# Kernel optimization log

Hardware: AMD Instinct MI355X
Metric: run time of the kernel (lower is better)

## Reference

```python
import jax, jax.numpy as jnp
import numpy as np

BATCH, SEQ, IN_DIM = 4, 2048, 4
D_MODEL, HEADS, D_HEAD = 128, 8, 16
DEPTH, BUCKET, N_HASHES = 6, 64, 8
D_FF = 4 * D_MODEL
NUM_CLASSES = 2
NB = SEQ // BUCKET          # 32 buckets per hash round
SELF_ATTN_VALUE = -5e4      # lucidrains TOKEN_SELF_ATTN_VALUE


def setup_inputs() -> dict:
    key = jax.random.key(0)
    ks = jax.random.split(key, 12)
    rn = lambda k, s: jax.random.normal(k, s, jnp.float32) * 0.02
    return {
        "x": jax.random.normal(ks[0], (BATCH, SEQ, IN_DIM), jnp.float32),
        "emb_W": rn(ks[1], (IN_DIM, D_MODEL)),
        "emb_b": jnp.zeros((D_MODEL,), jnp.float32),
        "Wqk": rn(ks[2], (DEPTH, D_MODEL, D_MODEL)),
        "Wv": rn(ks[3], (DEPTH, D_MODEL, D_MODEL)),
        "Wo": rn(ks[4], (DEPTH, D_MODEL, D_MODEL)),
        "R": jax.random.normal(ks[5], (DEPTH, HEADS, D_HEAD, N_HASHES, NB // 2), jnp.float32),
        "ln1_g": jnp.ones((DEPTH, D_MODEL), jnp.float32),
        "ln1_b": jnp.zeros((DEPTH, D_MODEL), jnp.float32),
        "ln2_g": jnp.ones((DEPTH, D_MODEL), jnp.float32),
        "ln2_b": jnp.zeros((DEPTH, D_MODEL), jnp.float32),
        "ff_W1": rn(ks[6], (DEPTH, D_MODEL, D_FF)),
        "ff_b1": jnp.zeros((DEPTH, D_FF), jnp.float32),
        "ff_W2": rn(ks[7], (DEPTH, D_FF, D_MODEL)),
        "ff_b2": jnp.zeros((DEPTH, D_MODEL), jnp.float32),
        "fc_W": rn(ks[8], (D_MODEL, NUM_CLASSES)),
        "fc_b": jnp.zeros((NUM_CLASSES,), jnp.float32),
    }


def layer_norm(x, g, b, eps=1e-5):
    m = x.mean(-1, keepdims=True)
    v = ((x - m) ** 2).mean(-1, keepdims=True)
    return (x - m) * jax.lax.rsqrt(v + eps) * g + b


def lsh_attention(x, wqk, wv, wo, rot):
    # x: [B,S,D]; rot: [H, dh, n_hashes, NB//2]. Shared-QK LSH attention (eval mode, no dropout).
    B, S, D = x.shape
    qk = (x @ wqk).reshape(B, S, HEADS, D_HEAD).transpose(0, 2, 1, 3)  # [B,H,S,dh]
    v = (x @ wv).reshape(B, S, HEADS, D_HEAD).transpose(0, 2, 1, 3)

    # --- hashing: argmax over [xR; -xR] rotations ---
    rx = jnp.einsum('bhsd,hdnr->bhnsr', qk, rot)                # [B,H,n_hashes,S,NB/2]
    buckets = jnp.argmax(jnp.concatenate([rx, -rx], -1), -1)    # [B,H,n_hashes,S] in [0,NB)
    buckets = buckets + (jnp.arange(N_HASHES) * NB)[None, None, :, None]
    buckets = buckets.reshape(B, HEADS, N_HASHES * S)

    # --- stable sort by (bucket, position) ---
    ticker = jnp.arange(N_HASHES * S)
    sticker = jnp.argsort(buckets * S + (ticker % S), axis=-1)   # [B,H,L]
    undo = jnp.argsort(sticker, axis=-1)
    st = sticker % S                                              # original positions

    sqk = jnp.take_along_axis(qk, st[..., None], axis=2)          # [B,H,L,dh]
    sv = jnp.take_along_axis(v, st[..., None], axis=2)

    n_chunks = N_HASHES * NB
    bq = sqk.reshape(B, HEADS, n_chunks, BUCKET, D_HEAD)
    bk = bq / jnp.linalg.norm(bq, axis=-1, keepdims=True)         # shared-QK: keys are normalized queries
    bv = sv.reshape(B, HEADS, n_chunks, BUCKET, D_HEAD)
    bt = st.reshape(B, HEADS, n_chunks, BUCKET)

    look_back = lambda t: jnp.concatenate([t, jnp.roll(t, 1, axis=2)], axis=3)
    bk, bv, bkt = look_back(bk), look_back(bv), look_back(bt)

    dots = jnp.einsum('bhcid,bhcjd->bhcij', bq, bk) * (D_HEAD ** -0.5)  # [B,H,C,64,128]
    dots = jnp.where(bt[..., :, None] == bkt[..., None, :], SELF_ATTN_VALUE, dots)

    logsum = jax.nn.logsumexp(dots, axis=-1)                      # [B,H,C,64]
    probs = jnp.exp(dots - logsum[..., None])
    bo = jnp.einsum('bhcij,bhcjd->bhcid', probs, bv)

    so = bo.reshape(B, HEADS, N_HASHES * S, D_HEAD)
    slog = logsum.reshape(B, HEADS, N_HASHES * S)
    o = jnp.take_along_axis(so, undo[..., None], axis=2).reshape(B, HEADS, N_HASHES, S, D_HEAD)
    logits = jnp.take_along_axis(slog, undo, axis=2).reshape(B, HEADS, N_HASHES, S, 1)

    w = jax.nn.softmax(logits, axis=2)                            # combine hash rounds
    out = (o * w).sum(axis=2)                                     # [B,H,S,dh]
    out = out.transpose(0, 2, 1, 3).reshape(B, S, D)
    return out @ wo


def reference(x, emb_W, emb_b, Wqk, Wv, Wo, R, ln1_g, ln1_b, ln2_g, ln2_b,
              ff_W1, ff_b1, ff_W2, ff_b2, fc_W, fc_b):
    h = x @ emb_W + emb_b

    def layer(h, p):
        wqk, wv, wo, r, g1, b1g, g2, b2g, w1, bb1, w2, bb2 = p
        h = h + lsh_attention(layer_norm(h, g1, b1g), wqk, wv, wo, r)
        y = layer_norm(h, g2, b2g)
        h = h + (jax.nn.gelu(y @ w1 + bb1) @ w2 + bb2)
        return h, None

    h, _ = jax.lax.scan(layer, h, (Wqk, Wv, Wo, R, ln1_g, ln1_b, ln2_g, ln2_b,
                                   ff_W1, ff_b1, ff_W2, ff_b2))
    return h.mean(axis=1) @ fc_W + fc_b
```

## Files before the change

kernel.cpp:

```cpp
#include <hip/hip_runtime.h>
#include <math.h>

#define BB 4
#define SS 2048
#define INDIM 4
#define DD 128
#define HH 8
#define DH 16
#define DEPTH 6
#define BUCKET 64
#define NHASH 8
#define NBK 32
#define DFF 512
#define LL (NHASH*SS)
#define NCHUNK (NHASH*NBK)
#define NBH (BB*HH)

typedef short bf16x8 __attribute__((ext_vector_type(8)));
typedef _Float16 f16x8 __attribute__((ext_vector_type(8)));
typedef _Float16 f16x2 __attribute__((ext_vector_type(2)));
typedef float f32x4 __attribute__((ext_vector_type(4)));

__device__ __forceinline__ unsigned short f2bf(float f) {
    unsigned u = __builtin_bit_cast(unsigned, f);
    unsigned r = u + 0x7FFFu + ((u >> 16) & 1u);
    return (unsigned short)(r >> 16);
}

__global__ void k_embed(const float* __restrict__ x, const float* __restrict__ W,
                        const float* __restrict__ b, float* __restrict__ h) {
    int idx = blockIdx.x * blockDim.x + threadIdx.x;
    if (idx >= BB*SS*DD) return;
    int d = idx % DD, bs = idx / DD;
    const float* xr = x + bs*INDIM;
    float acc = b[d];
    #pragma unroll
    for (int k = 0; k < INDIM; k++) acc += xr[k] * W[k*DD + d];
    h[idx] = acc;
}

__global__ void k_wcast(const float* __restrict__ src, unsigned short* __restrict__ dst,
                        int R, int C) {
    __shared__ float tile[32][33];
    int l = blockIdx.z;
    const float* s = src + (size_t)l*R*C;
    unsigned short* d = dst + (size_t)l*R*C;
    int c0 = blockIdx.x*32, r0 = blockIdx.y*32;
    int tx = threadIdx.x, ty = threadIdx.y;
    #pragma unroll
    for (int i = 0; i < 4; i++)
        tile[ty + i*8][tx] = s[(size_t)(r0 + ty + i*8)*C + c0 + tx];
    __syncthreads();
    #pragma unroll
    for (int i = 0; i < 4; i++)
        d[(size_t)(c0 + ty + i*8)*R + r0 + tx] = f2bf(tile[tx][ty + i*8]);
}

__global__ void k_wcast16(const float* __restrict__ src, _Float16* __restrict__ dst,
                          int R, int C) {
    __shared__ float tile[32][33];
    int l = blockIdx.z;
    const float* s = src + (size_t)l*R*C;
    _Float16* d = dst + (size_t)l*R*C;
    int c0 = blockIdx.x*32, r0 = blockIdx.y*32;
    int tx = threadIdx.x, ty = threadIdx.y;
    #pragma unroll
    for (int i = 0; i < 4; i++)
        tile[ty + i*8][tx] = s[(size_t)(r0 + ty + i*8)*C + c0 + tx];
    __syncthreads();
    #pragma unroll
    for (int i = 0; i < 4; i++)
        d[(size_t)(c0 + ty + i*8)*R + r0 + tx] = (_Float16)tile[tx][ty + i*8];
}

__global__ __launch_bounds__(256, 4)
void k_proj_qkv(const float* __restrict__ hin, const float* __restrict__ lng,
                const float* __restrict__ lnb, const _Float16* __restrict__ WqkT,
                const _Float16* __restrict__ WvT, float* __restrict__ qk,
                _Float16* __restrict__ kn16, _Float16* __restrict__ v16,
                float* __restrict__ nrmg) {
    __shared__ float A[16][128];
    __shared__ __align__(16) _Float16 Lf[16][136];
    int row0 = blockIdx.x * 16;
    int t = threadIdx.x;
    {
        const float4* src = (const float4*)(hin + (size_t)row0*DD);
        float4* dst = (float4*)&A[0][0];
        dst[t]       = src[t];
        dst[t + 256] = src[t + 256];
    }
    __syncthreads();
    {
        int r = t >> 4, sub = t & 15;
        float4 xa = *(const float4*)&A[r][sub*8];
        float4 xb = *(const float4*)&A[r][sub*8 + 4];
        float s = xa.x+xa.y+xa.z+xa.w + xb.x+xb.y+xb.z+xb.w;
        s += __shfl_xor(s,1); s += __shfl_xor(s,2);
        s += __shfl_xor(s,4); s += __shfl_xor(s,8);
        float m = s * (1.0f/128.0f);
        float d0=xa.x-m, d1=xa.y-m, d2=xa.z-m, d3=xa.w-m;
        float d4=xb.x-m, d5=xb.y-m, d6=xb.z-m, d7=xb.w-m;
        float vs = d0*d0+d1*d1+d2*d2+d3*d3+d4*d4+d5*d5+d6*d6+d7*d7;
        vs += __shfl_xor(vs,1); vs += __shfl_xor(vs,2);
        vs += __shfl_xor(vs,4); vs += __shfl_xor(vs,8);
        float inv = 1.0f / sqrtf(vs * (1.0f/128.0f) + 1e-5f);
        float4 ga = *(const float4*)&lng[sub*8], gb = *(const float4*)&lng[sub*8+4];
        float4 ba = *(const float4*)&lnb[sub*8], bb = *(const float4*)&lnb[sub*8+4];
        f16x8 vv;
        vv[0] = (_Float16)(d0*inv*ga.x + ba.x);
        vv[1] = (_Float16)(d1*inv*ga.y + ba.y);
        vv[2] = (_Float16)(d2*inv*ga.z + ba.z);
        vv[3] = (_Float16)(d3*inv*ga.w + ba.w);
        vv[4] = (_Float16)(d4*inv*gb.x + bb.x);
        vv[5] = (_Float16)(d5*inv*gb.y + bb.y);
        vv[6] = (_Float16)(d6*inv*gb.z + bb.z);
        vv[7] = (_Float16)(d7*inv*gb.w + bb.w);
        *(f16x8*)&Lf[r][sub*8] = vv;
    }
    __syncthreads();
    int w = t >> 6, lane = t & 63;
    int fr = lane & 15, kg = lane >> 4;
    f32x4 aq[2], av[2];
    aq[0] = (f32x4){0.f,0.f,0.f,0.f}; aq[1] = (f32x4){0.f,0.f,0.f,0.f};
    av[0] = (f32x4){0.f,0.f,0.f,0.f}; av[1] = (f32x4){0.f,0.f,0.f,0.f};
    #pragma unroll
    for (int ks = 0; ks < 4; ks++) {
        f16x8 af = *(const f16x8*)&Lf[fr][ks*32 + kg*8];
        #pragma unroll
        for (int nt = 0; nt < 2; nt++) {
            const _Float16* bp = WqkT + (size_t)(w*32 + nt*16 + fr)*128 + ks*32 + kg*8;
            f16x8 bq = *(const f16x8*)bp;
            aq[nt] = __builtin_amdgcn_mfma_f32_16x16x32_f16(af, bq, aq[nt], 0, 0, 0);
            const _Float16* vp = WvT + (size_t)(w*32 + nt*16 + fr)*128 + ks*32 + kg*8;
            f16x8 bv = *(const f16x8*)vp;
            av[nt] = __builtin_amdgcn_mfma_f32_16x16x32_f16(af, bv, av[nt], 0, 0, 0);
        }
    }
    int b = row0 / SS;
    int sb = row0 & (SS-1);
    #pragma unroll
    for (int nt = 0; nt < 2; nt++) {
        int n = w*32 + nt*16 + fr;
        int h_ = n >> 4, d_ = n & 15;
        float ssq[4];
        #pragma unroll
        for (int i = 0; i < 4; i++) { float xx = aq[nt][i]; ssq[i] = xx*xx; }
        #pragma unroll
        for (int o = 1; o <= 8; o <<= 1) {
            #pragma unroll
            for (int i = 0; i < 4; i++) ssq[i] += __shfl_xor(ssq[i], o);
        }
        #pragma unroll
        for (int i = 0; i < 4; i++) {
            int s = sb + kg*4 + i;
            size_t rowi = ((size_t)(b*HH + h_))*SS + s;
            qk[rowi*DH + d_] = aq[nt][i];
            float nn = sqrtf(ssq[i]);
            float inv = 1.0f / nn;
            kn16[rowi*DH + d_] = (_Float16)(aq[nt][i] * inv);
            v16[rowi*DH + d_]  = (_Float16)(av[nt][i]);
            if (d_ == 0) nrmg[rowi] = nn * 0.25f * 1.4426950408889634f;
        }
    }
}

__global__ void k_hash(const float* __restrict__ qk, const float* __restrict__ R,
                       int* __restrict__ bkt) {
    __shared__ float Rs[256];
    int idx = blockIdx.x*256 + threadIdx.x;
    int s = idx & (SS-1); int t2 = idx >> 11;
    int n = t2 & 7; int bh = t2 >> 3; int h_ = bh & 7;
    {
        int tt = threadIdx.x;
        int d = tt >> 4, r = tt & 15;
        Rs[tt] = R[(((h_*DH + d)*NHASH + n)*16) + r];
    }
    __syncthreads();
    const float4* q4 = (const float4*)(qk + ((size_t)bh*SS + s)*DH);
    float4 q0 = q4[0], q1 = q4[1], q2 = q4[2], q3 = q4[3];
    float rxv[16];
    #pragma unroll
    for (int r = 0; r < 16; r++) {
        rxv[r] = q0.x*Rs[  0+r] + q0.y*Rs[ 16+r] + q0.z*Rs[ 32+r] + q0.w*Rs[ 48+r]
               + q1.x*Rs[ 64+r] + q1.y*Rs[ 80+r] + q1.z*Rs[ 96+r] + q1.w*Rs[112+r]
               + q2.x*Rs[128+r] + q2.y*Rs[144+r] + q2.z*Rs[160+r] + q2.w*Rs[176+r]
               + q3.x*Rs[192+r] + q3.y*Rs[208+r] + q3.z*Rs[224+r] + q3.w*Rs[240+r];
    }
    float best = rxv[0]; int bi = 0;
    #pragma unroll
    for (int jx = 1; jx < 16; jx++) if (rxv[jx]  > best) { best = rxv[jx];  bi = jx; }
    #pragma unroll
    for (int jx = 0; jx < 16; jx++) if (-rxv[jx] > best) { best = -rxv[jx]; bi = 16 + jx; }
    bkt[idx] = n*NBK + bi;
}

__global__ void k_scatter(const int* __restrict__ bkt, int* __restrict__ sticker) {
    __shared__ int hist[256*33];
    __shared__ int cs[8*33];
    __shared__ int bbk[NBK];
    int blk = blockIdx.x;
    int n = blk & 7, bh = blk >> 3;
    int t = threadIdx.x;
    #pragma unroll
    for (int k = 0; k < NBK; k++) hist[t*33 + k] = 0;
    const int* bp = bkt + (size_t)bh*LL + n*SS;
    int local[8];
    #pragma unroll
    for (int e = 0; e < 8; e++) {
        int k = bp[t*8 + e] - n*NBK;
        local[e] = k;
        hist[t*33 + k]++;
    }
    __syncthreads();
    {
        int i = t >> 5, k = t & 31;
        int ssum = 0;
        #pragma unroll
        for (int rr = 0; rr < 32; rr++) ssum += hist[(i*32+rr)*33 + k];
        cs[i*33 + k] = ssum;
    }
    __syncthreads();
    if (t < 32) {
        int tot = 0;
        #pragma unroll
        for (int i = 0; i < 8; i++) tot += cs[i*33 + t];
        int x = tot;
        #pragma unroll
        for (int o = 1; o < 32; o <<= 1) {
            int y = __shfl(x, (t >= o) ? (t - o) : 0, 64);
            if (t >= o) x += y;
        }
        bbk[t] = n*SS + x - tot;
    }
    __syncthreads();
    {
        int i = t >> 5, k = t & 31;
        int run = bbk[k];
        for (int ii = 0; ii < i; ii++) run += cs[ii*33 + k];
        for (int rr = 0; rr < 32; rr++) {
            int idx = (i*32+rr)*33 + k;
            int c0 = hist[idx];
            hist[idx] = run;
            run += c0;
        }
    }
    __syncthreads();
    #pragma unroll
    for (int e = 0; e < 8; e++) {
        int k = local[e];
        int pos = hist[t*33 + k]++;
        sticker[(size_t)bh*LL + pos] = n*SS + t*8 + e;
    }
}

__global__ __launch_bounds__(256, 4)
void k_attn(const _Float16* __restrict__ kn16, const _Float16* __restrict__ v16,
            const float* __restrict__ nrmg, const int* __restrict__ sticker,
            _Float16* __restrict__ so, float* __restrict__ slog) {
    __shared__ __align__(16) char smem[33024];
    _Float16 (*Kf)[40]  = (_Float16(*)[40])smem;
    _Float16 (*P)[136]  = (_Float16(*)[136])(smem + 10240);
    _Float16 (*VT)[136] = (_Float16(*)[136])(smem + 27648);
    int*   pk   = (int*)(smem + 32000);
    float* nrm  = (float*)(smem + 32512);
    int*   lraw = (int*)(smem + 32768);

    int blk = blockIdx.x;
    int c = blk & (NCHUNK-1), bh = blk >> 8;
    int t = threadIdx.x;
    const int* stk = sticker + (size_t)bh*LL;

    if (t < 128) {
        int j = t;
        int cc = (j < 64) ? c : ((c + NCHUNK - 1) & (NCHUNK-1));
        int raw = stk[cc*BUCKET + (j & 63)];
        int sk = raw & (SS-1);
        const f16x8* kp = (const f16x8*)(kn16 + ((size_t)bh*SS + sk)*DH);
        f16x8 z = {0,0,0,0,0,0,0,0};
        *(f16x8*)&Kf[j][0]  = kp[0];
        *(f16x8*)&Kf[j][8]  = kp[1];
        *(f16x8*)&Kf[j][16] = z;
        *(f16x8*)&Kf[j][24] = z;
        pk[j] = sk;
        if (j < 64) { nrm[j] = nrmg[(size_t)bh*SS + sk]; lraw[j] = raw; }
    } else {
        int j = t - 128;
        int cc = (j < 64) ? c : ((c + NCHUNK - 1) & (NCHUNK-1));
        int sk = stk[cc*BUCKET + (j & 63)] & (SS-1);
        const f16x8* vp = (const f16x8*)(v16 + ((size_t)bh*SS + sk)*DH);
        f16x8 v0 = vp[0], v1 = vp[1];
        VT[ 0][j]=v0[0]; VT[ 1][j]=v0[1]; VT[ 2][j]=v0[2]; VT[ 3][j]=v0[3];
        VT[ 4][j]=v0[4]; VT[ 5][j]=v0[5]; VT[ 6][j]=v0[6]; VT[ 7][j]=v0[7];
        VT[ 8][j]=v1[0]; VT[ 9][j]=v1[1]; VT[10][j]=v1[2]; VT[11][j]=v1[3];
        VT[12][j]=v1[4]; VT[13][j]=v1[5]; VT[14][j]=v1[6]; VT[15][j]=v1[7];
    }
    __syncthreads();

    int w = t >> 6, lane = t & 63;
    int fr = lane & 15, kg = lane >> 4;
    int qrow = w*16 + fr;

    f32x4 acc[8];
    #pragma unroll
    for (int nt = 0; nt < 8; nt++) acc[nt] = (f32x4){0.f,0.f,0.f,0.f};
    {
        f16x8 kfq = *(const f16x8*)&Kf[qrow][kg*8];
        _Float16 qs = (_Float16)nrm[qrow];
        f16x8 bq = kfq * qs;
        #pragma unroll
        for (int nt = 0; nt < 8; nt++) {
            f16x8 afk = *(const f16x8*)&Kf[nt*16 + fr][kg*8];
            acc[nt] = __builtin_amdgcn_mfma_f32_16x16x32_f16(afk, bq, acc[nt], 0, 0, 0);
        }
    }
    int pq_self = pk[qrow];
    float s = 0.f;
    #pragma unroll
    for (int nt = 0; nt < 8; nt++) {
        int4 pk4 = *(const int4*)&pk[nt*16 + kg*4];
        float d0 = (pk4.x == pq_self) ? -5e4f : acc[nt][0];
        float d1 = (pk4.y == pq_self) ? -5e4f : acc[nt][1];
        float d2 = (pk4.z == pq_self) ? -5e4f : acc[nt][2];
        float d3 = (pk4.w == pq_self) ? -5e4f : acc[nt][3];
        float p0 = exp2f(d0), p1 = exp2f(d1), p2 = exp2f(d2), p3 = exp2f(d3);
        s += (p0 + p1) + (p2 + p3);
        f16x2 w0 = {(_Float16)p0, (_Float16)p1};
        f16x2 w1 = {(_Float16)p2, (_Float16)p3};
        *(f16x2*)&P[qrow][nt*16 + kg*4]     = w0;
        *(f16x2*)&P[qrow][nt*16 + kg*4 + 2] = w1;
    }
    s += __shfl_xor(s, 16);
    s += __shfl_xor(s, 32);
    if (kg == 0) slog[(size_t)bh*LL + lraw[qrow]] = __logf(s);

    f32x4 oacc = (f32x4){0.f,0.f,0.f,0.f};
    #pragma unroll
    for (int ks = 0; ks < 4; ks++) {
        f16x8 af = *(const f16x8*)&P[w*16 + fr][ks*32 + kg*8];
        f16x8 bf = *(const f16x8*)&VT[fr][ks*32 + kg*8];
        oacc = __builtin_amdgcn_mfma_f32_16x16x32_f16(af, bf, oacc, 0, 0, 0);
    }
    {
        int4 lr4 = *(const int4*)&lraw[w*16 + kg*4];
        so[((size_t)bh*LL + lr4.x)*DH + fr] = (_Float16)oacc[0];
        so[((size_t)bh*LL + lr4.y)*DH + fr] = (_Float16)oacc[1];
        so[((size_t)bh*LL + lr4.z)*DH + fr] = (_Float16)oacc[2];
        so[((size_t)bh*LL + lr4.w)*DH + fr] = (_Float16)oacc[3];
    }
}

__global__ __launch_bounds__(256, 3)
void k_out_ffn(const _Float16* __restrict__ so, const float* __restrict__ slog,
               const _Float16* __restrict__ WoT, const float* __restrict__ lng,
               const float* __restrict__ lnb, const unsigned short* __restrict__ W1T,
               const float* __restrict__ b1, const unsigned short* __restrict__ W2T,
               const float* __restrict__ b2, float* __restrict__ h) {
    __shared__ float hs[16][128];
    __shared__ __align__(16) _Float16 At[16][136];
    __shared__ __align__(16) unsigned short Albf[16][136];
    __shared__ __align__(16) unsigned short albf[16][520];
    int row0 = blockIdx.x * 16;
    int t = threadIdx.x;
    int b = row0 / SS;
    int s0 = row0 & (SS-1);

    {
        const float4* src = (const float4*)(h + (size_t)row0*DD);
        float4* dst = (float4*)&hs[0][0];
        dst[t]       = src[t];
        dst[t + 256] = src[t + 256];
    }
    {
        int half = t & 1, task = t >> 1;
        int r = task >> 3, h_ = task & 7;
        int s = s0 + r;
        int bh = b*HH + h_;
        const float* sl = slog + (size_t)bh*LL + s;
        float lg[NHASH];
        float m = -3.4e38f;
        #pragma unroll
        for (int n = 0; n < NHASH; n++) {
            lg[n] = sl[n*SS];
            m = fmaxf(m, lg[n]);
        }
        float S = 0.f;
        #pragma unroll
        for (int n = 0; n < NHASH; n++) S += __expf(lg[n] - m);
        float scale = __expf(-m) / S;
        float o[8] = {0,0,0,0,0,0,0,0};
        #pragma unroll
        for (int n = 0; n < NHASH; n++) {
            const f16x8* sp = (const f16x8*)(so + ((size_t)bh*LL + n*SS + s)*DH + half*8);
            f16x8 a = *sp;
            #pragma unroll
            for (int j = 0; j < 8; j++) o[j] += (float)a[j];
        }
        f16x8 ov;
        #pragma unroll
        for (int j = 0; j < 8; j++) ov[j] = (_Float16)(o[j] * scale);
        *(f16x8*)&At[r][h_*16 + half*8] = ov;
    }
    __syncthreads();

    int w = t >> 6, lane = t & 63;
    int fr = lane & 15, kg = lane >> 4;

    {
        f32x4 ao[2];
        ao[0] = (f32x4){0.f,0.f,0.f,0.f}; ao[1] = (f32x4){0.f,0.f,0.f,0.f};
        #pragma unroll
        for (int ks = 0; ks < 4; ks++) {
            f16x8 af = *(const f16x8*)&At[fr][ks*32 + kg*8];
            #pragma unroll
            for (int nt = 0; nt < 2; nt++) {
                const _Float16* bp = WoT + (size_t)(w*32 + nt*16 + fr)*128 + ks*32 + kg*8;
                f16x8 bf = *(const f16x8*)bp;
                ao[nt] = __builtin_amdgcn_mfma_f32_16x16x32_f16(af, bf, ao[nt], 0, 0, 0);
            }
        }
        #pragma unroll
        for (int nt = 0; nt < 2; nt++)
            #pragma unroll
            for (int i = 0; i < 4; i++)
                hs[kg*4 + i][w*32 + nt*16 + fr] += ao[nt][i];
    }
    __syncthreads();

    {
        int r = t >> 4, sub = t & 15;
        float4 xa = *(const float4*)&hs[r][sub*8];
        float4 xb = *(const float4*)&hs[r][sub*8 + 4];
        float s = xa.x+xa.y+xa.z+xa.w + xb.x+xb.y+xb.z+xb.w;
        s += __shfl_xor(s,1); s += __shfl_xor(s,2);
        s += __shfl_xor(s,4); s += __shfl_xor(s,8);
        float m = s * (1.0f/128.0f);
        float d0=xa.x-m, d1=xa.y-m, d2=xa.z-m, d3=xa.w-m;
        float d4=xb.x-m, d5=xb.y-m, d6=xb.z-m, d7=xb.w-m;
        float vs = d0*d0+d1*d1+d2*d2+d3*d3+d4*d4+d5*d5+d6*d6+d7*d7;
        vs += __shfl_xor(vs,1); vs += __shfl_xor(vs,2);
        vs += __shfl_xor(vs,4); vs += __shfl_xor(vs,8);
        float inv = 1.0f / sqrtf(vs * (1.0f/128.0f) + 1e-5f);
        float4 ga = *(const float4*)&lng[sub*8], gb = *(const float4*)&lng[sub*8+4];
        float4 ba = *(const float4*)&lnb[sub*8], bb = *(const float4*)&lnb[sub*8+4];
        bf16x8 vv;
        vv[0] = (short)f2bf(d0*inv*ga.x + ba.x);
        vv[1] = (short)f2bf(d1*inv*ga.y + ba.y);
        vv[2] = (short)f2bf(d2*inv*ga.z + ba.z);
        vv[3] = (short)f2bf(d3*inv*ga.w + ba.w);
        vv[4] = (short)f2bf(d4*inv*gb.x + bb.x);
        vv[5] = (short)f2bf(d5*inv*gb.y + bb.y);
        vv[6] = (short)f2bf(d6*inv*gb.z + bb.z);
        vv[7] = (short)f2bf(d7*inv*gb.w + bb.w);
        *(bf16x8*)&Albf[r][sub*8] = vv;
    }
    __syncthreads();

    f32x4 acc1[8];
    #pragma unroll
    for (int i = 0; i < 8; i++) acc1[i] = (f32x4){0.f, 0.f, 0.f, 0.f};
    {
        const unsigned short* w1p = W1T + (size_t)(w*128 + fr)*128 + kg*8;
        #pragma unroll
        for (int ks = 0; ks < 4; ks++) {
            bf16x8 af = *(const bf16x8*)&Albf[fr][ks*32 + kg*8];
            #pragma unroll
            for (int nt = 0; nt < 8; nt++) {
                bf16x8 bf = *(const bf16x8*)(w1p + nt*16*128 + ks*32);
                acc1[nt] = __builtin_amdgcn_mfma_f32_16x16x32_bf16(af, bf, acc1[nt], 0, 0, 0);
            }
        }
    }
    #pragma unroll
    for (int nt = 0; nt < 8; nt++) {
        int col = w*128 + nt*16 + fr;
        float bias = b1[col];
        #pragma unroll
        for (int i = 0; i < 4; i++) {
            int row = kg*4 + i;
            float x = acc1[nt][i] + bias;
            float t0 = tanhf(0.7978845608028654f * (x + 0.044715f*x*x*x));
            albf[row][col] = f2bf(0.5f*x*(1.0f + t0));
        }
    }
    __syncthreads();

    f32x4 acc2[2];
    acc2[0] = (f32x4){0.f,0.f,0.f,0.f};
    acc2[1] = (f32x4){0.f,0.f,0.f,0.f};
    {
        const unsigned short* w2p = W2T + (size_t)(w*32 + fr)*512 + kg*8;
        #pragma unroll
        for (int ks = 0; ks < 16; ks++) {
            bf16x8 af = *(const bf16x8*)&albf[fr][ks*32 + kg*8];
            bf16x8 b0 = *(const bf16x8*)(w2p + ks*32);
            bf16x8 b1f = *(const bf16x8*)(w2p + 16*512 + ks*32);
            acc2[0] = __builtin_amdgcn_mfma_f32_16x16x32_bf16(af, b0, acc2[0], 0, 0, 0);
            acc2[1] = __builtin_amdgcn_mfma_f32_16x16x32_bf16(af, b1f, acc2[1], 0, 0, 0);
        }
    }
    #pragma unroll
    for (int nt = 0; nt < 2; nt++) {
        int col = w*32 + nt*16 + fr;
        float bias = b2[col];
        #pragma unroll
        for (int i = 0; i < 4; i++) {
            int row = kg*4 + i;
            h[(size_t)(row0 + row)*DD + col] = hs[row][col] + acc2[nt][i] + bias;
        }
    }
}

__global__ void k_pool(const float* __restrict__ h, float* __restrict__ partial) {
    int blk = blockIdx.x;
    int t = threadIdx.x;
    int b = blk >> 6, c = blk & 63;
    const float* hp = h + ((size_t)b*SS + c*32)*DD + t;
    float acc = 0.f;
    #pragma unroll
    for (int i = 0; i < 32; i++) acc += hp[i*DD];
    partial[blk*DD + t] = acc;
}

__global__ void k_final(const float* __restrict__ partial, const float* __restrict__ fcW,
                        const float* __restrict__ fcb, float* __restrict__ out) {
    __shared__ float red[4];
    int b = blockIdx.x, t = threadIdx.x;
    const float* pp = partial + (size_t)b*64*DD + t;
    float acc = 0.f;
    #pragma unroll
    for (int c = 0; c < 64; c++) acc += pp[c*DD];
    float pooled = acc * (1.0f/(float)SS);
    float p0 = pooled * fcW[t*2+0];
    float p1 = pooled * fcW[t*2+1];
    #pragma unroll
    for (int o = 32; o >= 1; o >>= 1) { p0 += __shfl_xor(p0,o); p1 += __shfl_xor(p1,o); }
    int w = t >> 6;
    if ((t & 63) == 0) { red[w*2] = p0; red[w*2+1] = p1; }
    __syncthreads();
    if (t == 0) {
        out[b*2 + 0] = red[0] + red[2] + fcb[0];
        out[b*2 + 1] = red[1] + red[3] + fcb[1];
    }
}

extern "C" void kernel_launch(void* const* d_in, const int* in_sizes, int n_in,
                              void* d_out, int out_size, void* d_ws, size_t ws_size,
                              hipStream_t stream) {
    const float* x    = (const float*)d_in[0];
    const float* embW = (const float*)d_in[1];
    const float* embB = (const float*)d_in[2];
    const float* Wqk  = (const float*)d_in[3];
    const float* Wv   = (const float*)d_in[4];
    const float* Wo   = (const float*)d_in[5];
    const float* R    = (const float*)d_in[6];
    const float* ln1g = (const float*)d_in[7];
    const float* ln1b = (const float*)d_in[8];
    const float* ln2g = (const float*)d_in[9];
    const float* ln2b = (const float*)d_in[10];
    const float* W1   = (const float*)d_in[11];
    const float* b1   = (const float*)d_in[12];
    const float* W2   = (const float*)d_in[13];
    const float* b2   = (const float*)d_in[14];
    const float* fcW  = (const float*)d_in[15];
    const float* fcb  = (const float*)d_in[16];
    float* out = (float*)d_out;

    char* w = (char*)d_ws;
    auto carve = [&](size_t bytes) -> char* {
        char* p = w;
        w += (bytes + 255) & ~(size_t)255;
        return p;
    };
    float* h       = (float*)carve((size_t)BB*SS*DD*4);
    float* qk      = (float*)carve((size_t)NBH*SS*DH*4);
    _Float16* kn16 = (_Float16*)carve((size_t)NBH*SS*DH*2);
    _Float16* v16  = (_Float16*)carve((size_t)NBH*SS*DH*2);
    float* nrmg    = (float*)carve((size_t)NBH*SS*4);
    int*   bkt     = (int*)  carve((size_t)NBH*LL*4);
    int*   sticker = (int*)  carve((size_t)NBH*LL*4);
    _Float16* so   = (_Float16*)carve((size_t)NBH*LL*DH*2);
    float* slog    = (float*)carve((size_t)NBH*LL*4);
    float* partial = (float*)carve((size_t)BB*64*DD*4);
    unsigned short* w1t = (unsigned short*)carve((size_t)DEPTH*DD*DFF*2);
    unsigned short* w2t = (unsigned short*)carve((size_t)DEPTH*DFF*DD*2);
    _Float16* wqk16 = (_Float16*)carve((size_t)DEPTH*DD*DD*2);
    _Float16* wv16  = (_Float16*)carve((size_t)DEPTH*DD*DD*2);
    _Float16* wo16  = (_Float16*)carve((size_t)DEPTH*DD*DD*2);

    k_wcast<<<dim3(DFF/32, DD/32, DEPTH), dim3(32, 8), 0, stream>>>(W1, w1t, DD, DFF);
    k_wcast<<<dim3(DD/32, DFF/32, DEPTH), dim3(32, 8), 0, stream>>>(W2, w2t, DFF, DD);
    k_wcast16<<<dim3(DD/32, DD/32, DEPTH), dim3(32, 8), 0, stream>>>(Wqk, wqk16, DD, DD);
    k_wcast16<<<dim3(DD/32, DD/32, DEPTH), dim3(32, 8), 0, stream>>>(Wv, wv16, DD, DD);
    k_wcast16<<<dim3(DD/32, DD/32, DEPTH), dim3(32, 8), 0, stream>>>(Wo, wo16, DD, DD);

    k_embed<<<(BB*SS*DD)/256, 256, 0, stream>>>(x, embW, embB, h);

    for (int l = 0; l < DEPTH; l++) {
        const _Float16* wqkl = wqk16 + (size_t)l*DD*DD;
        const _Float16* wvl  = wv16  + (size_t)l*DD*DD;
        const _Float16* wol  = wo16  + (size_t)l*DD*DD;
        const float* rl  = R   + (size_t)l*HH*DH*NHASH*16;
        const float* g1  = ln1g + l*DD; const float* bg1 = ln1b + l*DD;
        const float* g2  = ln2g + l*DD; const float* bg2 = ln2b + l*DD;
        const unsigned short* w1l = w1t + (size_t)l*DD*DFF;
        const unsigned short* w2l = w2t + (size_t)l*DFF*DD;
        const float* bb1 = b1 + l*DFF;
        const float* bb2 = b2 + l*DD;

        k_proj_qkv<<<(BB*SS)/16, 256, 0, stream>>>(h, g1, bg1, wqkl, wvl,
                                                   qk, kn16, v16, nrmg);
        k_hash<<<(NBH*NHASH*SS)/256, 256, 0, stream>>>(qk, rl, bkt);
        k_scatter<<<NBH*NHASH, 256, 0, stream>>>(bkt, sticker);
        k_attn<<<NBH*NCHUNK, 256, 0, stream>>>(kn16, v16, nrmg, sticker, so, slog);
        k_out_ffn<<<(BB*SS)/16, 256, 0, stream>>>(so, slog, wol, g2, bg2,
                                                  w1l, bb1, w2l, bb2, h);
    }

    k_pool<<<BB*64, 128, 0, stream>>>(h, partial);
    k_final<<<BB, 128, 0, stream>>>(partial, fcW, fcb, out);
}
```

Measured before the change: 513.4 us.

## Hash from normalized fp16 keys, drop fp32 qk buffer, shrink attention LDS

Drops the fp32 qk intermediate. The hash kernel now reads the normalized fp16 keys, because argmax over rotations does not change when the vector is positively scaled. The attention kernel stops zero-padding the K tile in shared memory to 32 columns: it pads with registers when kg>=2 and raises launch_bounds occupancy from 4 to 5. The goal is less global traffic and better occupancy, at the cost of fp16 rounding in the hash input, which can flip near-tie buckets.

```diff
diff --git a/kernel.cpp b/kernel.cpp
--- a/kernel.cpp
+++ b/kernel.cpp
@@ -76,7 +76,7 @@
 __global__ __launch_bounds__(256, 4)
 void k_proj_qkv(const float* __restrict__ hin, const float* __restrict__ lng,
                 const float* __restrict__ lnb, const _Float16* __restrict__ WqkT,
-                const _Float16* __restrict__ WvT, float* __restrict__ qk,
+                const _Float16* __restrict__ WvT,
                 _Float16* __restrict__ kn16, _Float16* __restrict__ v16,
                 float* __restrict__ nrmg) {
     __shared__ float A[16][128];
@@ -154,7 +154,6 @@
         for (int i = 0; i < 4; i++) {
             int s = sb + kg*4 + i;
             size_t rowi = ((size_t)(b*HH + h_))*SS + s;
-            qk[rowi*DH + d_] = aq[nt][i];
             float nn = sqrtf(ssq[i]);
             float inv = 1.0f / nn;
             kn16[rowi*DH + d_] = (_Float16)(aq[nt][i] * inv);
@@ -164,7 +163,7 @@
     }
 }
 
-__global__ void k_hash(const float* __restrict__ qk, const float* __restrict__ R,
+__global__ void k_hash(const _Float16* __restrict__ kn16, const float* __restrict__ R,
                        int* __restrict__ bkt) {
     __shared__ float Rs[256];
     int idx = blockIdx.x*256 + threadIdx.x;
@@ -176,15 +175,18 @@
         Rs[tt] = R[(((h_*DH + d)*NHASH + n)*16) + r];
     }
     __syncthreads();
-    const float4* q4 = (const float4*)(qk + ((size_t)bh*SS + s)*DH);
-    float4 q0 = q4[0], q1 = q4[1], q2 = q4[2], q3 = q4[3];
+    const f16x8* q8 = (const f16x8*)(kn16 + ((size_t)bh*SS + s)*DH);
+    f16x8 qa = q8[0], qb = q8[1];
+    float q[16];
+    #pragma unroll
+    for (int j = 0; j < 8; j++) { q[j] = (float)qa[j]; q[8+j] = (float)qb[j]; }
     float rxv[16];
     #pragma unroll
     for (int r = 0; r < 16; r++) {
-        rxv[r] = q0.x*Rs[  0+r] + q0.y*Rs[ 16+r] + q0.z*Rs[ 32+r] + q0.w*Rs[ 48+r]
-               + q1.x*Rs[ 64+r] + q1.y*Rs[ 80+r] + q1.z*Rs[ 96+r] + q1.w*Rs[112+r]
-               + q2.x*Rs[128+r] + q2.y*Rs[144+r] + q2.z*Rs[160+r] + q2.w*Rs[176+r]
-               + q3.x*Rs[192+r] + q3.y*Rs[208+r] + q3.z*Rs[224+r] + q3.w*Rs[240+r];
+        float acc = 0.f;
+        #pragma unroll
+        for (int d = 0; d < 16; d++) acc += q[d] * Rs[d*16 + r];
+        rxv[r] = acc;
     }
     float best = rxv[0]; int bi = 0;
     #pragma unroll
@@ -253,17 +255,17 @@
     }
 }
 
-__global__ __launch_bounds__(256, 4)
+__global__ __launch_bounds__(256, 5)
 void k_attn(const _Float16* __restrict__ kn16, const _Float16* __restrict__ v16,
             const float* __restrict__ nrmg, const int* __restrict__ sticker,
             _Float16* __restrict__ so, float* __restrict__ slog) {
-    __shared__ __align__(16) char smem[33024];
-    _Float16 (*Kf)[40]  = (_Float16(*)[40])smem;
-    _Float16 (*P)[136]  = (_Float16(*)[136])(smem + 10240);
-    _Float16 (*VT)[136] = (_Float16(*)[136])(smem + 27648);
-    int*   pk   = (int*)(smem + 32000);
-    float* nrm  = (float*)(smem + 32512);
-    int*   lraw = (int*)(smem + 32768);
+    __shared__ __align__(16) char smem[28928];
+    _Float16 (*Kf)[24]  = (_Float16(*)[24])smem;
+    _Float16 (*P)[136]  = (_Float16(*)[136])(smem + 6144);
+    _Float16 (*VT)[136] = (_Float16(*)[136])(smem + 23552);
+    int*   pk   = (int*)(smem + 27904);
+    float* nrm  = (float*)(smem + 28416);
+    int*   lraw = (int*)(smem + 28672);
 
     int blk = blockIdx.x;
     int c = blk & (NCHUNK-1), bh = blk >> 8;
@@ -276,11 +278,8 @@
         int raw = stk[cc*BUCKET + (j & 63)];
         int sk = raw & (SS-1);
         const f16x8* kp = (const f16x8*)(kn16 + ((size_t)bh*SS + sk)*DH);
-        f16x8 z = {0,0,0,0,0,0,0,0};
-        *(f16x8*)&Kf[j][0]  = kp[0];
-        *(f16x8*)&Kf[j][8]  = kp[1];
-        *(f16x8*)&Kf[j][16] = z;
-        *(f16x8*)&Kf[j][24] = z;
+        *(f16x8*)&Kf[j][0] = kp[0];
+        *(f16x8*)&Kf[j][8] = kp[1];
         pk[j] = sk;
         if (j < 64) { nrm[j] = nrmg[(size_t)bh*SS + sk]; lraw[j] = raw; }
     } else {
@@ -304,12 +303,17 @@
     #pragma unroll
     for (int nt = 0; nt < 8; nt++) acc[nt] = (f32x4){0.f,0.f,0.f,0.f};
     {
-        f16x8 kfq = *(const f16x8*)&Kf[qrow][kg*8];
-        _Float16 qs = (_Float16)nrm[qrow];
-        f16x8 bq = kfq * qs;
+        f16x8 z = {0,0,0,0,0,0,0,0};
+        f16x8 bq = z;
+        if (kg < 2) {
+            f16x8 kfq = *(const f16x8*)&Kf[qrow][kg*8];
+            _Float16 qs = (_Float16)nrm[qrow];
+            bq = kfq * qs;
+        }
         #pragma unroll
         for (int nt = 0; nt < 8; nt++) {
-            f16x8 afk = *(const f16x8*)&Kf[nt*16 + fr][kg*8];
+            f16x8 afk = z;
+            if (kg < 2) afk = *(const f16x8*)&Kf[nt*16 + fr][kg*8];
             acc[nt] = __builtin_amdgcn_mfma_f32_16x16x32_f16(afk, bq, acc[nt], 0, 0, 0);
         }
     }
@@ -572,7 +576,6 @@
         return p;
     };
     float* h       = (float*)carve((size_t)BB*SS*DD*4);
-    float* qk      = (float*)carve((size_t)NBH*SS*DH*4);
     _Float16* kn16 = (_Float16*)carve((size_t)NBH*SS*DH*2);
     _Float16* v16  = (_Float16*)carve((size_t)NBH*SS*DH*2);
     float* nrmg    = (float*)carve((size_t)NBH*SS*4);
@@ -608,8 +611,8 @@
         const float* bb2 = b2 + l*DD;
 
         k_proj_qkv<<<(BB*SS)/16, 256, 0, stream>>>(h, g1, bg1, wqkl, wvl,
-                                                   qk, kn16, v16, nrmg);
-        k_hash<<<(NBH*NHASH*SS)/256, 256, 0, stream>>>(qk, rl, bkt);
+                                                   kn16, v16, nrmg);
+        k_hash<<<(NBH*NHASH*SS)/256, 256, 0, stream>>>(kn16, rl, bkt);
         k_scatter<<<NBH*NHASH, 256, 0, stream>>>(bkt, sticker);
         k_attn<<<NBH*NCHUNK, 256, 0, stream>>>(kn16, v16, nrmg, sticker, so, slog);
         k_out_ffn<<<(BB*SS)/16, 256, 0, stream>>>(so, slog, wol, g2, bg2,
```

Result: slower. 845.8 us (+64.8%).
